# Kernel tuning notes

Hardware: AMD Instinct MI355X
Metric: run time of the kernel (lower is better)

## Reference

```python
import jax, jax.numpy as jnp
import numpy as np
from jax import lax


def _interp_matrix(n_in: int, n_out: int) -> jnp.ndarray:
    """Row-stochastic [n_out, n_in] matrix for 1-D linear interp, align_corners=True."""
    if n_in == 1:
        return jnp.ones((n_out, 1), dtype=jnp.float32)
    pos = jnp.arange(n_out, dtype=jnp.float32) * ((n_in - 1) / (n_out - 1))
    lo = jnp.clip(jnp.floor(pos).astype(jnp.int32), 0, n_in - 2)
    frac = pos - lo.astype(jnp.float32)
    rows = jnp.arange(n_out)
    W = jnp.zeros((n_out, n_in), dtype=jnp.float32)
    W = W.at[rows, lo].add(1.0 - frac)
    W = W.at[rows, lo + 1].add(frac)
    return W


def setup_inputs() -> dict:
    key = jax.random.key(0)
    ks = jax.random.split(key, 10)
    B, C, H, W = 8, 64, 128, 128
    Ch = C // 2
    x = jax.random.normal(ks[0], (B, C, H, W), dtype=jnp.float32)
    # fan-in scaled weights to keep softmax logits in a sane range
    pool_w = jax.random.normal(ks[1], (C, C, 3, 3), dtype=jnp.float32) / np.sqrt(C * 9)
    pool_b = jax.random.normal(ks[2], (C,), dtype=jnp.float32) * 0.1
    q_w = jax.random.normal(ks[3], (Ch, C), dtype=jnp.float32) / np.sqrt(C)
    q_b = jax.random.normal(ks[4], (Ch,), dtype=jnp.float32) * 0.1
    k_w = jax.random.normal(ks[5], (Ch, C), dtype=jnp.float32) / np.sqrt(C)
    k_b = jax.random.normal(ks[6], (Ch,), dtype=jnp.float32) * 0.1
    v_w = jax.random.normal(ks[7], (C, C), dtype=jnp.float32) / np.sqrt(C)
    v_b = jax.random.normal(ks[8], (C,), dtype=jnp.float32) * 0.1
    gamma = jax.random.normal(ks[9], (1,), dtype=jnp.float32)
    return {"x": x, "pool_w": pool_w, "pool_b": pool_b, "q_w": q_w, "q_b": q_b,
            "k_w": k_w, "k_b": k_b, "v_w": v_w, "v_b": v_b, "gamma": gamma}


def reference(x, pool_w, pool_b, q_w, q_b, k_w, k_b, v_w, v_b, gamma):
    # 3x3 stride-2 pad-1 conv (the 'pool')
    xp = lax.conv_general_dilated(x, pool_w, window_strides=(2, 2),
                                  padding=((1, 1), (1, 1)),
                                  dimension_numbers=('NCHW', 'OIHW', 'NCHW'))
    xp = xp + pool_b[None, :, None, None]
    B, C, h, w = xp.shape
    N = h * w
    xf = xp.reshape(B, C, N)  # [B, C, N]
    # 1x1 convs as matmuls over the channel dim
    q = jnp.einsum('oc,bcn->bon', q_w, xf) + q_b[None, :, None]   # [B, C/2, N]
    k = jnp.einsum('oc,bcn->bon', k_w, xf) + k_b[None, :, None]   # [B, C/2, N]
    v = jnp.einsum('oc,bcn->bon', v_w, xf) + v_b[None, :, None]   # [B, C, N]
    # energy[b, n, m] = <q[:, n], k[:, m]>  -> softmax over m
    energy = jnp.einsum('bdn,bdm->bnm', q, k)                     # [B, N, N]
    attn = jax.nn.softmax(energy, axis=-1)
    # out = value @ attention^T  (torch: bmm(v, attn.permute(0,2,1)))
    out = jnp.einsum('bcm,bnm->bcn', v, attn).reshape(B, C, h, w)
    out = gamma[0] * out
    # bilinear upsample to input size, align_corners=True (separable matmuls)
    H, Wd = x.shape[2], x.shape[3]
    Wh = _interp_matrix(h, H)
    Ww = _interp_matrix(w, Wd)
    out = jnp.einsum('Hh,bchw->bcHw', Wh, out)
    out = jnp.einsum('Ww,bchw->bchW', Ww, out)
    return out + x
```

## Files before the change

kernel.cpp:

```cpp
#include <hip/hip_runtime.h>


typedef __attribute__((ext_vector_type(8))) short bf16x8;
typedef __attribute__((ext_vector_type(4))) float f32x4;

#define DEV static __device__ __forceinline__

DEV unsigned f2bf(float f) {
  union { float f; unsigned u; } a; a.f = f;
  return (a.u + 0x7FFFu + ((a.u >> 16) & 1u)) >> 16;
}
DEV float u2f(unsigned u) { union { unsigned u; float f; } a; a.u = u; return a.f; }
DEV unsigned cvtpk(float lo, float hi) {
  unsigned r;
  asm("v_cvt_pk_bf16_f32 %0, %1, %2" : "=v"(r) : "v"(lo), "v"(hi));
  return r;
}
DEV bf16x8 mk_bf16x8(unsigned w0, unsigned w1, unsigned w2, unsigned w3) {
  union { unsigned u[4]; bf16x8 v; } x;
  x.u[0] = w0; x.u[1] = w1; x.u[2] = w2; x.u[3] = w3;
  return x.v;
}
DEV void gload_lds16(const void* g, void* l) {
  __builtin_amdgcn_global_load_lds(
      (const __attribute__((address_space(1))) void*)g,
      (__attribute__((address_space(3))) void*)l, 16, 0, 0);
}

__global__ __launch_bounds__(256) void prep_kernel(
    const float* __restrict__ pw, const float* __restrict__ qw,
    const float* __restrict__ kw, const float* __restrict__ vw,
    const float* __restrict__ qb, const float* __restrict__ kb,
    const float* __restrict__ vb,
    unsigned short* __restrict__ Ag, unsigned short* __restrict__ A2g,
    float* __restrict__ bias2) {
  const float LOG2E = 1.4426950408889634f;
  const int i = blockIdx.x * 256 + threadIdx.x;
  if (i < 36864) {
    const int oc = i / 576, k = i - oc * 576;
    const int tap = k >> 6, ic = k & 63;
    Ag[i] = (unsigned short)f2bf(pw[(oc * 64 + ic) * 9 + tap]);
  }
  const int j = i - 36864;
  if (j >= 0 && j < 8192) {
    const int r = j >> 6, c = j & 63;
    if (r < 32)       A2g[j] = (unsigned short)f2bf(qw[r * 64 + c] * LOG2E);
    else if (r < 64)  A2g[j] = (unsigned short)f2bf(kw[(r - 32) * 64 + c]);
    else              A2g[j] = (unsigned short)f2bf(vw[(r - 64) * 64 + c]);
  }
  if (j >= 8192 && j < 8320) {
    const int r = j - 8192;
    bias2[r] = r < 32 ? qb[r] * LOG2E : (r < 64 ? kb[r - 32] : vb[r - 64]);
  }
}

__global__ __launch_bounds__(256) void convqkv_kernel(
    const float* __restrict__ x, const unsigned short* __restrict__ Ag,
    const float* __restrict__ pool_b, const unsigned short* __restrict__ A2g,
    const float* __restrict__ bias2,
    unsigned short* __restrict__ qT, unsigned short* __restrict__ kT,
    unsigned short* __restrict__ vM) {
  const int b = blockIdx.x >> 6, oy = blockIdx.x & 63;
  const int t = threadIdx.x, w = t >> 6, lane = t & 63;
  const int lr = lane & 15, lg = lane >> 4;
  __shared__ unsigned short sIn[390 * 64];
  __shared__ unsigned short sXP[64 * 64];
  char* sInB = (char*)sIn;
  char* sXPB = (char*)sXP;

  bf16x8 af[18];
  {
    const unsigned short* ap = Ag + (w * 16 + lr) * 576 + (lg << 3);
    #pragma unroll
    for (int kc = 0; kc < 18; ++kc)
      af[kc] = *(const bf16x8*)(ap + kc * 32);
  }

  #pragma unroll
  for (int rr = 0; rr < 2; ++rr) {
    const int pos = t + rr * 256;
    if (pos < 390) {
      const int ky = pos / 130, xi = pos - ky * 130;
      const int iy = 2 * oy + ky - 1, ix = xi - 1;
      const bool ok = (iy >= 0) & (iy < 128) & (ix >= 0) & (ix < 128);
      const float* xs = x + ((size_t)(b * 64) * 128 + (ok ? iy : 0)) * 128 +
                        (ok ? ix : 0);
      const int sw = pos & 7;
      #pragma unroll
      for (int o = 0; o < 8; ++o) {
        float f[8];
        #pragma unroll
        for (int jj = 0; jj < 8; ++jj)
          f[jj] = ok ? xs[(size_t)(o * 8 + jj) * 16384] : 0.f;
        bf16x8 v = mk_bf16x8(cvtpk(f[0], f[1]), cvtpk(f[2], f[3]),
                             cvtpk(f[4], f[5]), cvtpk(f[6], f[7]));
        *(bf16x8*)(sInB + pos * 128 + ((o ^ sw) << 4)) = v;
      }
    }
  }
  __syncthreads();

  f32x4 acc[4];
  #pragma unroll
  for (int nt = 0; nt < 4; ++nt) acc[nt] = (f32x4){0.f, 0.f, 0.f, 0.f};
  #pragma unroll
  for (int kc = 0; kc < 18; ++kc) {
    const int tap = kc >> 1, ky = tap / 3, kx = tap - ky * 3;
    const int o = ((kc & 1) << 2) + lg;
    #pragma unroll
    for (int nt = 0; nt < 4; ++nt) {
      const int xi = 2 * (nt * 16 + lr) + kx;
      const int pos = ky * 130 + xi;
      bf16x8 bfr = *(const bf16x8*)(sInB + pos * 128 + ((o ^ (pos & 7)) << 4));
      acc[nt] = __builtin_amdgcn_mfma_f32_16x16x32_bf16(af[kc], bfr, acc[nt],
                                                        0, 0, 0);
    }
  }

  const int ocBase = w * 16 + (lg << 2);
  float pb[4];
  #pragma unroll
  for (int r = 0; r < 4; ++r) pb[r] = pool_b[ocBase + r];
  const int ocOct = ocBase >> 3;
  const int withinB = (ocBase & 7) * 2;
  #pragma unroll
  for (int nt = 0; nt < 4; ++nt) {
    const int pos = nt * 16 + lr;
    const unsigned p01 = cvtpk(acc[nt][0] + pb[0], acc[nt][1] + pb[1]);
    const unsigned p23 = cvtpk(acc[nt][2] + pb[2], acc[nt][3] + pb[3]);
    char* base = sXPB + pos * 128 + ((ocOct ^ (pos & 7)) << 4) + withinB;
    *(unsigned*)(base) = p01;
    *(unsigned*)(base + 4) = p23;
  }
  __syncthreads();

  bf16x8 a2[2][2];
  #pragma unroll
  for (int mt = 0; mt < 2; ++mt)
    #pragma unroll
    for (int kc2 = 0; kc2 < 2; ++kc2)
      a2[mt][kc2] = *(const bf16x8*)(A2g + ((2 * w + mt) * 16 + lr) * 64 +
                                     kc2 * 32 + (lg << 3));
  f32x4 acc2[2][4];
  #pragma unroll
  for (int mt = 0; mt < 2; ++mt)
    #pragma unroll
    for (int nt = 0; nt < 4; ++nt) acc2[mt][nt] = (f32x4){0.f, 0.f, 0.f, 0.f};
  #pragma unroll
  for (int kc2 = 0; kc2 < 2; ++kc2) {
    const int o2 = (kc2 << 2) + lg;
    #pragma unroll
    for (int nt = 0; nt < 4; ++nt) {
      const int pos = nt * 16 + lr;
      bf16x8 bfr = *(const bf16x8*)(sXPB + pos * 128 + ((o2 ^ (pos & 7)) << 4));
      acc2[0][nt] = __builtin_amdgcn_mfma_f32_16x16x32_bf16(a2[0][kc2], bfr,
                                                            acc2[0][nt], 0, 0, 0);
      acc2[1][nt] = __builtin_amdgcn_mfma_f32_16x16x32_bf16(a2[1][kc2], bfr,
                                                            acc2[1][nt], 0, 0, 0);
    }
  }

  const int n0g = oy << 6;
  #pragma unroll
  for (int mt = 0; mt < 2; ++mt) {
    const int rowB = (2 * w + mt) * 16 + (lg << 2);
    float b2[4];
    #pragma unroll
    for (int r = 0; r < 4; ++r) b2[r] = bias2[rowB + r];
    if (rowB < 32) {
      #pragma unroll
      for (int nt = 0; nt < 4; ++nt) {
        const int n = n0g + nt * 16 + lr;
        unsigned* dst = (unsigned*)(qT + (((size_t)(b << 12) + n) << 5) + rowB);
        dst[0] = cvtpk(acc2[mt][nt][0] + b2[0], acc2[mt][nt][1] + b2[1]);
        dst[1] = cvtpk(acc2[mt][nt][2] + b2[2], acc2[mt][nt][3] + b2[3]);
      }
    } else if (rowB < 64) {
      #pragma unroll
      for (int nt = 0; nt < 4; ++nt) {
        const int n = n0g + nt * 16 + lr;
        unsigned* dst = (unsigned*)(kT + (((size_t)(b << 12) + n) << 5) + rowB - 32);
        dst[0] = cvtpk(acc2[mt][nt][0] + b2[0], acc2[mt][nt][1] + b2[1]);
        dst[1] = cvtpk(acc2[mt][nt][2] + b2[2], acc2[mt][nt][3] + b2[3]);
      }
    } else {
      const int cv = rowB - 64;
      #pragma unroll
      for (int nt = 0; nt < 4; ++nt) {
        const int n = n0g + nt * 16 + lr;
        #pragma unroll
        for (int r = 0; r < 4; ++r)
          vM[(((size_t)(b << 6) + cv + r) << 12) + n] =
              (unsigned short)f2bf(acc2[mt][nt][r] + b2[r]);
      }
    }
  }
}

template <int NSPLIT>
__global__ __launch_bounds__(256, 2) void attn_kernel(
    const unsigned short* __restrict__ qT, const unsigned short* __restrict__ kT,
    const unsigned short* __restrict__ vM,
    unsigned short* __restrict__ Pb, float* __restrict__ Lbuf) {
  constexpr int CH = 64 / NSPLIT;
  __shared__ char lds[24576];
  __shared__ char Plds[4][4608];
  const int t = threadIdx.x, w = t >> 6, lane = t & 63;
  const int lr = lane & 15, lg = lane >> 4;
  const int b = blockIdx.x & 7;
  const int u = (blockIdx.x >> 3) & 15;
  const int s = blockIdx.x >> 7;
  const int n0 = (u << 8) + (w << 6);
  const int kb0 = s * (CH << 6);
  char* Pw = Plds[w];

  bf16x8 bq[4];
  #pragma unroll
  for (int nt = 0; nt < 4; ++nt)
    bq[nt] = *(const bf16x8*)(
        qT + (((size_t)(b << 12) + n0 + nt * 16 + lr) << 5) + (lg << 3));

  const unsigned short* ksrc = kT + ((size_t)b << 17);
  const unsigned short* vsrcb = vM + ((size_t)b << 18);

  f32x4 acc[4][4];
  #pragma unroll
  for (int nt = 0; nt < 4; ++nt)
    #pragma unroll
    for (int ct = 0; ct < 4; ++ct) acc[nt][ct] = (f32x4){0.f, 0.f, 0.f, 0.f};
  float l_run[4] = {0.f, 0.f, 0.f, 0.f};

  const int vsw = (lane & 7) ^ ((lane >> 3) & 7);
  const int klocal = (w << 4) + (lane >> 2);
  const int kseg = (lane & 3) ^ ((klocal >> 1) & 3);

  #define STAGE(ci_) {                                                         \
    const int kb_ = kb0 + (((ci_) & (CH - 1)) << 6);                           \
    char* sb_ = lds + ((ci_) & 1) * 12288;                                     \
    gload_lds16((const void*)(ksrc + (((size_t)(kb_ + klocal)) << 5) +         \
                  (kseg << 3)),                                                \
                sb_ + (w << 10));                                              \
    gload_lds16((const void*)(vsrcb +                                          \
                  (((size_t)((w << 4) + (lane >> 3))) << 12) + kb_ +           \
                  (vsw << 3)),                                                 \
                sb_ + 4096 + (w << 11));                                       \
    gload_lds16((const void*)(vsrcb +                                          \
                  (((size_t)((w << 4) + 8 + (lane >> 3))) << 12) + kb_ +       \
                  (vsw << 3)),                                                 \
                sb_ + 4096 + (w << 11) + 1024);                                \
  }

  STAGE(0);

  for (int cc = 0; cc < CH; ++cc) {
    asm volatile("s_waitcnt vmcnt(0)" ::: "memory");
    __builtin_amdgcn_s_barrier();
    __builtin_amdgcn_sched_barrier(0);
    if (cc + 1 < CH) STAGE(cc + 1);
    char* base = lds + (cc & 1) * 12288;

    #pragma unroll
    for (int p = 0; p < 2; ++p) {
      f32x4 st[2][4];
      const f32x4 z4 = {0.f, 0.f, 0.f, 0.f};
      __builtin_amdgcn_s_setprio(1);
      #pragma unroll
      for (int j = 0; j < 4; ++j) {
        const int key = 16 * j + lr;
        const bf16x8 ka = *(const bf16x8*)(
            base + (key << 6) + ((lg ^ ((key >> 1) & 3)) << 4));
        st[0][j] = __builtin_amdgcn_mfma_f32_16x16x32_bf16(ka, bq[2 * p], z4,
                                                           0, 0, 0);
        st[1][j] = __builtin_amdgcn_mfma_f32_16x16x32_bf16(ka, bq[2 * p + 1],
                                                           z4, 0, 0, 0);
      }
      __builtin_amdgcn_s_setprio(0);

      #pragma unroll
      for (int q = 0; q < 2; ++q) {
        float ps0 = 0.f, ps1 = 0.f;
        #pragma unroll
        for (int j = 0; j < 4; ++j) {
          const float p0 = __builtin_amdgcn_exp2f(st[q][j][0]);
          const float p1 = __builtin_amdgcn_exp2f(st[q][j][1]);
          const float p2 = __builtin_amdgcn_exp2f(st[q][j][2]);
          const float p3 = __builtin_amdgcn_exp2f(st[q][j][3]);
          ps0 += p0 + p1;
          ps1 += p2 + p3;
          *(uint2*)(Pw + (q * 16 + lr) * 144 + (((j << 2) + lg) << 3)) =
              (uint2){cvtpk(p0, p1), cvtpk(p2, p3)};
        }
        l_run[2 * p + q] += ps0 + ps1;
      }

      #pragma unroll
      for (int h = 0; h < 2; ++h) {
        bf16x8 vr[4];
        #pragma unroll
        for (int ct = 0; ct < 4; ++ct) {
          const int c = (ct << 4) + lr;
          const int o = (h << 2) + lg;
          vr[ct] = *(const bf16x8*)(base + 4096 + (c << 7) +
                                    ((o ^ (lr & 7)) << 4));
        }
        #pragma unroll
        for (int q = 0; q < 2; ++q) {
          const bf16x8 pbf = *(const bf16x8*)(
              Pw + (q * 16 + lr) * 144 + (((h << 3) + (lg << 1)) << 3));
          __builtin_amdgcn_s_setprio(1);
          #pragma unroll
          for (int ct = 0; ct < 4; ++ct)
            acc[2 * p + q][ct] = __builtin_amdgcn_mfma_f32_16x16x32_bf16(
                vr[ct], pbf, acc[2 * p + q][ct], 0, 0, 0);
          __builtin_amdgcn_s_setprio(0);
        }
      }
    }
  }

  #pragma unroll
  for (int nt = 0; nt < 4; ++nt) {
    l_run[nt] += __shfl_xor(l_run[nt], 16, 64);
    l_run[nt] += __shfl_xor(l_run[nt], 32, 64);
  }

  unsigned short* dst = Pb + ((size_t)s << 21);
  #pragma unroll
  for (int nt = 0; nt < 4; ++nt) {
    const int q = n0 + nt * 16 + lr;
    #pragma unroll
    for (int ct = 0; ct < 4; ++ct)
      #pragma unroll
      for (int r = 0; r < 4; ++r) {
        const int c = (ct << 4) + (lg << 2) + r;
        dst[((size_t)((b << 6) + c) << 12) + q] =
            (unsigned short)f2bf(acc[nt][ct][r]);
      }
  }
  if (lane < 16) {
    #pragma unroll
    for (int nt = 0; nt < 4; ++nt)
      Lbuf[((size_t)(s * 8 + b) << 12) + n0 + nt * 16 + lane] = l_run[nt];
  }
  #undef STAGE
}

template <int NSPLIT>
__global__ __launch_bounds__(256) void merge_upsample_kernel(
    const unsigned short* __restrict__ Pb, const float* __restrict__ Lbuf,
    const float* __restrict__ gamma_p, const float* __restrict__ x,
    float* __restrict__ out) {
  __shared__ float sA[4096];
  const int t = threadIdx.x;
  const int b = blockIdx.x >> 6, c = blockIdx.x & 63;
  const float g = gamma_p[0];
  const size_t basebc = ((size_t)((b << 6) + c) << 12);

  #pragma unroll
  for (int i = 0; i < 2; ++i) {
    const int n0 = (t + (i << 8)) << 3;
    float num[8] = {0.f, 0.f, 0.f, 0.f, 0.f, 0.f, 0.f, 0.f};
    #pragma unroll
    for (int s = 0; s < NSPLIT; ++s) {
      const uint4 v = *(const uint4*)(Pb + ((size_t)s << 21) + basebc + n0);
      num[0] += u2f(v.x << 16); num[1] += u2f(v.x & 0xffff0000u);
      num[2] += u2f(v.y << 16); num[3] += u2f(v.y & 0xffff0000u);
      num[4] += u2f(v.z << 16); num[5] += u2f(v.z & 0xffff0000u);
      num[6] += u2f(v.w << 16); num[7] += u2f(v.w & 0xffff0000u);
    }
    float den[8] = {0.f, 0.f, 0.f, 0.f, 0.f, 0.f, 0.f, 0.f};
    #pragma unroll
    for (int s = 0; s < NSPLIT; ++s) {
      const float* lp = Lbuf + (((size_t)(s * 8 + b)) << 12) + n0;
      const f32x4 l0 = *(const f32x4*)lp;
      const f32x4 l1 = *(const f32x4*)(lp + 4);
      #pragma unroll
      for (int j = 0; j < 4; ++j) { den[j] += l0[j]; den[4 + j] += l1[j]; }
    }
    #pragma unroll
    for (int j = 0; j < 8; ++j) sA[n0 + j] = g * num[j] / den[j];
  }
  __syncthreads();

  const float sr = 63.0f / 127.0f;
  const float* xb = x + (((size_t)((b << 6) + c)) << 14);
  float* ob = out + (((size_t)((b << 6) + c)) << 14);
  for (int k = 0; k < 16; ++k) {
    const int qid = t + (k << 8);
    const int Y = qid >> 5, X0 = (qid & 31) << 2;
    const float fy = Y * sr;
    int iy = (int)fy; if (iy > 62) iy = 62;
    const float ty = fy - (float)iy;
    const float* r0 = sA + iy * 64;
    const float* r1 = r0 + 64;
    float tmp[4];
    #pragma unroll
    for (int kk = 0; kk < 4; ++kk) {
      const int X = X0 + kk;
      const float fx = X * sr;
      int ix = (int)fx; if (ix > 62) ix = 62;
      const float tx = fx - (float)ix;
      const float v0 = r0[ix] + tx * (r0[ix + 1] - r0[ix]);
      const float v1 = r1[ix] + tx * (r1[ix + 1] - r1[ix]);
      tmp[kk] = v0 + ty * (v1 - v0);
    }
    const size_t o = ((size_t)Y << 7) + X0;
    const f32x4 xv = *(const f32x4*)(xb + o);
    f32x4 ov = {tmp[0] + xv[0], tmp[1] + xv[1], tmp[2] + xv[2], tmp[3] + xv[3]};
    *(f32x4*)(ob + o) = ov;
  }
}

extern "C" void kernel_launch(void* const* d_in, const int* in_sizes, int n_in,
                              void* d_out, int out_size, void* d_ws, size_t ws_size,
                              hipStream_t stream) {
  const float* x      = (const float*)d_in[0];
  const float* pool_w = (const float*)d_in[1];
  const float* pool_b = (const float*)d_in[2];
  const float* q_w    = (const float*)d_in[3];
  const float* q_b    = (const float*)d_in[4];
  const float* k_w    = (const float*)d_in[5];
  const float* k_b    = (const float*)d_in[6];
  const float* v_w    = (const float*)d_in[7];
  const float* v_b    = (const float*)d_in[8];
  const float* gamma  = (const float*)d_in[9];
  float* out = (float*)d_out;

  char* ws = (char*)d_ws;
  unsigned short* Ag   = (unsigned short*)(ws);
  unsigned short* A2g  = (unsigned short*)(ws + 81920);
  float* bias2         = (float*)(ws + 98304);
  unsigned short* qT   = (unsigned short*)(ws + 1048576);
  unsigned short* kT   = (unsigned short*)(ws + 3145728);
  unsigned short* vM   = (unsigned short*)(ws + 5242880);
  unsigned short* Pb   = (unsigned short*)(ws + 9437184);

  prep_kernel<<<177, 256, 0, stream>>>(pool_w, q_w, k_w, v_w, q_b, k_b, v_b,
                                       Ag, A2g, bias2);
  convqkv_kernel<<<512, 256, 0, stream>>>(x, Ag, pool_b, A2g, bias2, qT, kT, vM);

  if (ws_size >= 44040192u) {
    float* Lbuf = (float*)(ws + 9437184 + 8 * 4194304);
    attn_kernel<8><<<1024, 256, 0, stream>>>(qT, kT, vM, Pb, Lbuf);
    merge_upsample_kernel<8><<<512, 256, 0, stream>>>(Pb, Lbuf, gamma, x, out);
  } else {
    float* Lbuf = (float*)(ws + 9437184 + 4 * 4194304);
    attn_kernel<4><<<512, 256, 0, stream>>>(qT, kT, vM, Pb, Lbuf);
    merge_upsample_kernel<4><<<512, 256, 0, stream>>>(Pb, Lbuf, gamma, x, out);
  }
}
```

Measured before the change: 83.10 us.

## Reorder attention inner loop to split keys in halves across all query tiles

The inner chunk loop is restructured to iterate over two 32-key halves instead of two 32-query halves. Each half computes scores for all four query tiles, writes a smaller P buffer (row stride 72 instead of 144), and loads the V fragments once per half instead of once per query pair. This cuts redundant V LDS reads and shrinks the P staging footprint, but may raise register pressure because each half now holds eight score tiles alongside the full accumulator.

```diff
diff --git a/kernel.cpp b/kernel.cpp
--- a/kernel.cpp
+++ b/kernel.cpp
@@ -260,60 +260,56 @@
     char* base = lds + (cc & 1) * 12288;
 
     #pragma unroll
-    for (int p = 0; p < 2; ++p) {
-      f32x4 st[2][4];
+    for (int h = 0; h < 2; ++h) {
+      f32x4 st[4][2];
       const f32x4 z4 = {0.f, 0.f, 0.f, 0.f};
       __builtin_amdgcn_s_setprio(1);
       #pragma unroll
-      for (int j = 0; j < 4; ++j) {
-        const int key = 16 * j + lr;
+      for (int jp = 0; jp < 2; ++jp) {
+        const int key = (h << 5) + (jp << 4) + lr;
         const bf16x8 ka = *(const bf16x8*)(
             base + (key << 6) + ((lg ^ ((key >> 1) & 3)) << 4));
-        st[0][j] = __builtin_amdgcn_mfma_f32_16x16x32_bf16(ka, bq[2 * p], z4,
-                                                           0, 0, 0);
-        st[1][j] = __builtin_amdgcn_mfma_f32_16x16x32_bf16(ka, bq[2 * p + 1],
-                                                           z4, 0, 0, 0);
+        #pragma unroll
+        for (int nt = 0; nt < 4; ++nt)
+          st[nt][jp] = __builtin_amdgcn_mfma_f32_16x16x32_bf16(ka, bq[nt], z4,
+                                                               0, 0, 0);
       }
       __builtin_amdgcn_s_setprio(0);
 
       #pragma unroll
-      for (int q = 0; q < 2; ++q) {
-        float ps0 = 0.f, ps1 = 0.f;
+      for (int nt = 0; nt < 4; ++nt) {
+        float ps = 0.f;
         #pragma unroll
-        for (int j = 0; j < 4; ++j) {
-          const float p0 = __builtin_amdgcn_exp2f(st[q][j][0]);
-          const float p1 = __builtin_amdgcn_exp2f(st[q][j][1]);
-          const float p2 = __builtin_amdgcn_exp2f(st[q][j][2]);
-          const float p3 = __builtin_amdgcn_exp2f(st[q][j][3]);
-          ps0 += p0 + p1;
-          ps1 += p2 + p3;
-          *(uint2*)(Pw + (q * 16 + lr) * 144 + (((j << 2) + lg) << 3)) =
+        for (int jp = 0; jp < 2; ++jp) {
+          const float p0 = __builtin_amdgcn_exp2f(st[nt][jp][0]);
+          const float p1 = __builtin_amdgcn_exp2f(st[nt][jp][1]);
+          const float p2 = __builtin_amdgcn_exp2f(st[nt][jp][2]);
+          const float p3 = __builtin_amdgcn_exp2f(st[nt][jp][3]);
+          ps += (p0 + p1) + (p2 + p3);
+          *(uint2*)(Pw + (nt * 16 + lr) * 72 + (((jp << 2) + lg) << 3)) =
               (uint2){cvtpk(p0, p1), cvtpk(p2, p3)};
         }
-        l_run[2 * p + q] += ps0 + ps1;
-      }
-
-      #pragma unroll
-      for (int h = 0; h < 2; ++h) {
-        bf16x8 vr[4];
+        l_run[nt] += ps;
+      }
+
+      bf16x8 vr[4];
+      #pragma unroll
+      for (int ct = 0; ct < 4; ++ct) {
+        const int c = (ct << 4) + lr;
+        const int o = (h << 2) + lg;
+        vr[ct] = *(const bf16x8*)(base + 4096 + (c << 7) +
+                                  ((o ^ (lr & 7)) << 4));
+      }
+      #pragma unroll
+      for (int nt = 0; nt < 4; ++nt) {
+        const bf16x8 pbf =
+            *(const bf16x8*)(Pw + (nt * 16 + lr) * 72 + (lg << 4));
+        __builtin_amdgcn_s_setprio(1);
         #pragma unroll
-        for (int ct = 0; ct < 4; ++ct) {
-          const int c = (ct << 4) + lr;
-          const int o = (h << 2) + lg;
-          vr[ct] = *(const bf16x8*)(base + 4096 + (c << 7) +
-                                    ((o ^ (lr & 7)) << 4));
-        }
-        #pragma unroll
-        for (int q = 0; q < 2; ++q) {
-          const bf16x8 pbf = *(const bf16x8*)(
-              Pw + (q * 16 + lr) * 144 + (((h << 3) + (lg << 1)) << 3));
-          __builtin_amdgcn_s_setprio(1);
-          #pragma unroll
-          for (int ct = 0; ct < 4; ++ct)
-            acc[2 * p + q][ct] = __builtin_amdgcn_mfma_f32_16x16x32_bf16(
-                vr[ct], pbf, acc[2 * p + q][ct], 0, 0, 0);
-          __builtin_amdgcn_s_setprio(0);
-        }
+        for (int ct = 0; ct < 4; ++ct)
+          acc[nt][ct] = __builtin_amdgcn_mfma_f32_16x16x32_bf16(
+              vr[ct], pbf, acc[nt][ct], 0, 0, 0);
+        __builtin_amdgcn_s_setprio(0);
       }
     }
   }
```

Measured after the change: 98.32 us. +18.3%, slower.
